# Optimization experiments

Measured on AMD Instinct MI355X. Metric: run time of the kernel, lower is better.

## Reference

```python
import jax, jax.numpy as jnp
import numpy as np

N, TI, ENC_DIM, DEC_DIM, ATT_DIM = 32, 2000, 512, 512, 512


def setup_inputs() -> dict:
    key = jax.random.key(0)
    ks = jax.random.split(key, 8)
    enc_pad = jax.random.normal(ks[0], (N, TI, ENC_DIM), dtype=jnp.float32)
    dec_prev = jax.random.normal(ks[1], (N, DEC_DIM), dtype=jnp.float32)
    ali_prev = jax.random.uniform(ks[2], (N, TI), dtype=jnp.float32)
    # lengths in [Ti//2, Ti], force one full-length row (module uses max(enc_len) as mask width)
    enc_len = jax.random.randint(ks[3], (N,), TI // 2, TI + 1)
    enc_len = enc_len.at[0].set(TI)
    # learned params (nn.Linear layout: W [out, in])
    s_e = 1.0 / np.sqrt(ENC_DIM)
    s_d = 1.0 / np.sqrt(DEC_DIM)
    s_a = 1.0 / np.sqrt(ATT_DIM)
    W_enc = jax.random.uniform(ks[4], (ATT_DIM, ENC_DIM), minval=-s_e, maxval=s_e, dtype=jnp.float32)
    b_enc = jax.random.uniform(ks[5], (ATT_DIM,), minval=-s_e, maxval=s_e, dtype=jnp.float32)
    W_dec = jax.random.uniform(ks[6], (ATT_DIM, DEC_DIM), minval=-s_d, maxval=s_d, dtype=jnp.float32)
    w_v = jax.random.uniform(ks[7], (ATT_DIM,), minval=-s_a, maxval=s_a, dtype=jnp.float32)
    return {"enc_pad": enc_pad, "enc_len": enc_len, "dec_prev": dec_prev,
            "ali_prev": ali_prev, "W_enc": W_enc, "b_enc": b_enc,
            "W_dec": W_dec, "w_v": w_v}


def reference(enc_pad, enc_len, dec_prev, ali_prev, W_enc, b_enc, W_dec, w_v):
    # enc_part: N x Ti x A  (enc_proj with bias)
    enc_part = jnp.einsum('ntd,ad->nta', enc_pad, W_enc) + b_enc
    # dec_part: N x A  (dec_proj, no bias)
    dec_part = jnp.einsum('nd,ad->na', dec_prev, W_dec)
    # additive score e = w^T tanh(enc_part + dec_part): N x Ti
    e = jnp.einsum('nta,a->nt', jnp.tanh(enc_part + dec_part[:, None, :]), w_v)
    # padding mask: positions >= enc_len are masked
    mask = jnp.arange(e.shape[1]) >= enc_len[:, None]  # N x Ti
    e = jnp.where(mask, -jnp.inf, e)
    ali = jax.nn.softmax(e, axis=1)  # N x Ti
    ctx = jnp.einsum('nt,ntd->nd', ali, enc_pad)  # N x D_enc
    return (ali, ctx)
```

## Files before the change

### kernel.cpp

```cpp
#include <hip/hip_runtime.h>
#include <stdint.h>


#define NB  32
#define TI  2000
#define ED  512
#define AD  512
#define M_TOT (NB * TI)
#define NSPLIT 20
#define TCHUNK (TI / NSPLIT)
#define MTS 500
#define NKS 16

using f16x8 = __attribute__((ext_vector_type(8))) _Float16;
using f32x4 = __attribute__((ext_vector_type(4))) float;

#define GLD16(g, l)                                                     \
    __builtin_amdgcn_global_load_lds(                                   \
        (const __attribute__((address_space(1))) void*)(g),             \
        (__attribute__((address_space(3))) void*)(l), 16, 0, 0)

__device__ __forceinline__ float fast_tanh(float s) {
    s = fminf(fmaxf(s, -15.f), 15.f);
    float t = __expf(2.f * s);
    return __fdividef(t - 1.f, t + 1.f);
}

__device__ __forceinline__ f16x8 cvt8(float4 a, float4 b) {
    f16x8 h;
    h[0] = (_Float16)a.x; h[1] = (_Float16)a.y; h[2] = (_Float16)a.z; h[3] = (_Float16)a.w;
    h[4] = (_Float16)b.x; h[5] = (_Float16)b.y; h[6] = (_Float16)b.z; h[7] = (_Float16)b.w;
    return h;
}

__global__ void k_wconvert(const float* __restrict__ Wenc, _Float16* __restrict__ W16,
                           const float* __restrict__ dec_prev, const float* __restrict__ W_dec,
                           const float* __restrict__ b_enc, float* __restrict__ db) {
    __shared__ float xd[ED];
    int bx = blockIdx.x;
    int tid = threadIdx.x;
    if (bx >= 128) {
        int n = bx - 128;
        for (int k = tid; k < ED; k += 256) xd[k] = dec_prev[n * ED + k];
        __syncthreads();
        for (int a = tid; a < AD; a += 256) {
            const float* wr = W_dec + (size_t)a * ED;
            float s = 0.f;
#pragma unroll 8
            for (int k = 0; k < ED; k += 4) {
                float4 w = *(const float4*)(wr + k);
                s += xd[k] * w.x + xd[k + 1] * w.y + xd[k + 2] * w.z + xd[k + 3] * w.w;
            }
            db[n * AD + a] = s + b_enc[a];
        }
        return;
    }
    int idx = bx * 4096 + tid * 16;
    int ks  = idx >> 15;
    int r   = idx & 32767;
    int gk  = r >> 13;
    int a   = (r & 8191) >> 4;
    int k   = ks * 32 + gk * 8;
    const float* s = Wenc + (size_t)a * ED + k;
    float4 x0 = *(const float4*)s;
    float4 x1 = *(const float4*)(s + 4);
    *(f16x8*)((char*)W16 + idx) = cvt8(x0, x1);
}

__global__ void k_decdb(const float* __restrict__ dec_prev,
                        const float* __restrict__ W_dec,
                        const float* __restrict__ b_enc,
                        float* __restrict__ db) {
    int n = blockIdx.x;
    __shared__ float xd[ED];
    for (int k = threadIdx.x; k < ED; k += 256) xd[k] = dec_prev[n * ED + k];
    __syncthreads();
    for (int a = threadIdx.x; a < AD; a += 256) {
        const float* wr = W_dec + (size_t)a * ED;
        float s = 0.f;
#pragma unroll 8
        for (int k = 0; k < ED; k += 4) {
            float4 w = *(const float4*)(wr + k);
            s += xd[k] * w.x + xd[k + 1] * w.y + xd[k + 2] * w.z + xd[k + 3] * w.w;
        }
        db[n * AD + a] = s + b_enc[a];
    }
}

__launch_bounds__(512, 2)
__global__ void k_score256(const float* __restrict__ enc, const _Float16* __restrict__ W16,
                           const float* __restrict__ db, const float* __restrict__ wv,
                           float* __restrict__ e_out) {
    __shared__ alignas(16) char As0[16384];
    __shared__ alignas(16) char As1[16384];
    __shared__ alignas(16) char Bs0[32768];
    __shared__ alignas(16) char Bs1[32768];

    const int mt   = blockIdx.x;
    const int tid  = threadIdx.x;
    const int lane = tid & 63;
    const int w    = tid >> 6;
    const int wm   = w >> 2;
    const int wn   = w & 3;
    const int m0   = mt * 128;
    const int lr   = lane & 15;
    const int gk   = lane >> 4;

    const int srow = tid >> 3;
    const int sq   = (tid & 7) * 16;
    const int sqx  = (sq ^ ((srow & 7) << 4)) >> 2;
    const float* asrc = enc + (size_t)(m0 + srow) * ED + sqx;

    const char* wbase = (const char*)W16;

    f32x4 acc[4][8];
#pragma unroll
    for (int rb = 0; rb < 4; ++rb)
#pragma unroll
        for (int cb = 0; cb < 8; ++cb) acc[rb][cb] = (f32x4){0.f, 0.f, 0.f, 0.f};

#define STAGE(ks, dA, dB)                                               \
    {                                                                   \
        GLD16(asrc + (ks) * 32,            (dA) + tid * 16);            \
        GLD16(asrc + 64 * ED + (ks) * 32,  (dA) + 8192 + tid * 16);     \
        const char* wsl = wbase + ((ks) << 15);                         \
        GLD16(wsl + tid * 16,          (dB) + tid * 16);                \
        GLD16(wsl + 8192 + tid * 16,   (dB) + 8192 + tid * 16);         \
        GLD16(wsl + 16384 + tid * 16,  (dB) + 16384 + tid * 16);        \
        GLD16(wsl + 24576 + tid * 16,  (dB) + 24576 + tid * 16);        \
    }

#define COMPUTE(sA, sB)                                                          \
    {                                                                            \
        f16x8 aF[4], bF[8];                                                      \
        _Pragma("unroll")                                                        \
        for (int rb = 0; rb < 4; ++rb) {                                         \
            int row = wm * 64 + rb * 16 + lr;                                    \
            int b0  = row * 128 + gk * 32;                                       \
            int sw  = (row & 7) << 4;                                            \
            f32x4 lo = *(const f32x4*)((sA) + (b0 ^ sw));                        \
            f32x4 hi = *(const f32x4*)((sA) + ((b0 + 16) ^ sw));                 \
            f16x8 h;                                                             \
            h[0] = (_Float16)lo[0]; h[1] = (_Float16)lo[1];                      \
            h[2] = (_Float16)lo[2]; h[3] = (_Float16)lo[3];                      \
            h[4] = (_Float16)hi[0]; h[5] = (_Float16)hi[1];                      \
            h[6] = (_Float16)hi[2]; h[7] = (_Float16)hi[3];                      \
            aF[rb] = h;                                                          \
        }                                                                        \
        _Pragma("unroll")                                                        \
        for (int cb = 0; cb < 8; ++cb) {                                         \
            int brow = wn * 128 + cb * 16 + lr;                                  \
            bF[cb] = *(const f16x8*)((sB) + gk * 8192 + brow * 16);              \
        }                                                                        \
        __builtin_amdgcn_s_setprio(1);                                           \
        _Pragma("unroll")                                                        \
        for (int rb = 0; rb < 4; ++rb)                                           \
            _Pragma("unroll")                                                    \
            for (int cb = 0; cb < 8; ++cb)                                       \
                acc[rb][cb] = __builtin_amdgcn_mfma_f32_16x16x32_f16(            \
                    aF[rb], bF[cb], acc[rb][cb], 0, 0, 0);                       \
        __builtin_amdgcn_s_setprio(0);                                           \
    }

#define ITER(k, Ac, Bc, An, Bn)  STAGE(k + 1, An, Bn); COMPUTE(Ac, Bc); __syncthreads();

    STAGE(0, As0, Bs0); __syncthreads();
    ITER(0,  As0, Bs0, As1, Bs1)
    ITER(1,  As1, Bs1, As0, Bs0)
    ITER(2,  As0, Bs0, As1, Bs1)
    ITER(3,  As1, Bs1, As0, Bs0)
    ITER(4,  As0, Bs0, As1, Bs1)
    ITER(5,  As1, Bs1, As0, Bs0)
    ITER(6,  As0, Bs0, As1, Bs1)
    ITER(7,  As1, Bs1, As0, Bs0)
    ITER(8,  As0, Bs0, As1, Bs1)
    ITER(9,  As1, Bs1, As0, Bs0)
    ITER(10, As0, Bs0, As1, Bs1)
    ITER(11, As1, Bs1, As0, Bs0)
    ITER(12, As0, Bs0, As1, Bs1)
    ITER(13, As1, Bs1, As0, Bs0)
    ITER(14, As0, Bs0, As1, Bs1)
    COMPUTE(As1, Bs1); __syncthreads();
#undef ITER
#undef COMPUTE
#undef STAGE

    float* e_red = (float*)As0;
    float wvv[8];
#pragma unroll
    for (int cb = 0; cb < 8; ++cb) wvv[cb] = wv[wn * 128 + cb * 16 + lr];

#pragma unroll
    for (int rb = 0; rb < 4; ++rb) {
#pragma unroll
        for (int i = 0; i < 4; ++i) {
            int row_local = wm * 64 + rb * 16 + gk * 4 + i;
            int m = m0 + row_local;
            int n = m / TI;
            const float* dbp = db + (size_t)n * AD + wn * 128;
            float rs = 0.f;
#pragma unroll
            for (int cb = 0; cb < 8; ++cb) {
                float s = acc[rb][cb][i] + dbp[cb * 16 + lr];
                rs += fast_tanh(s) * wvv[cb];
            }
            rs += __shfl_xor(rs, 1);
            rs += __shfl_xor(rs, 2);
            rs += __shfl_xor(rs, 4);
            rs += __shfl_xor(rs, 8);
            if (lr == 0) e_red[wn * 128 + row_local] = rs;
        }
    }
    __syncthreads();
    if (tid < 128)
        e_out[m0 + tid] =
            e_red[tid] + e_red[128 + tid] + e_red[256 + tid] + e_red[384 + tid];
}

__launch_bounds__(256, 2)
__global__ void k_score_fb(const float* __restrict__ X, const float* __restrict__ W,
                           const float* __restrict__ db, const float* __restrict__ wv,
                           float* __restrict__ e_part) {
    __shared__ alignas(16) _Float16 Xs[128][72];
    __shared__ alignas(16) _Float16 Ws[128][72];
    __shared__ float e_red[2][128];

    const int tid = threadIdx.x, lane = tid & 63, wid = tid >> 6;
    const int wr = wid >> 1, wc = wid & 1;
    const int m0 = blockIdx.x * 128, a0 = blockIdx.y * 128;

    f32x4 acc[4][4];
#pragma unroll
    for (int rb = 0; rb < 4; ++rb)
#pragma unroll
        for (int cb = 0; cb < 4; ++cb) acc[rb][cb] = (f32x4){0.f, 0.f, 0.f, 0.f};

    const int lr = lane & 15;
    const int lk = (lane >> 4) << 3;

    for (int kt = 0; kt < ED; kt += 64) {
#pragma unroll
        for (int i = 0; i < 4; ++i) {
            int idx = tid + i * 256, r = idx >> 3, c = (idx & 7) << 3;
            const float* gx = X + (size_t)(m0 + r) * ED + kt + c;
            float4 x0 = *(const float4*)gx, x1 = *(const float4*)(gx + 4);
            *(f16x8*)&Xs[r][c] = cvt8(x0, x1);
            const float* gw = W + (size_t)(a0 + r) * ED + kt + c;
            float4 w0 = *(const float4*)gw, w1 = *(const float4*)(gw + 4);
            *(f16x8*)&Ws[r][c] = cvt8(w0, w1);
        }
        __syncthreads();
#pragma unroll
        for (int kb = 0; kb < 64; kb += 32) {
            f16x8 aF[4], bF[4];
#pragma unroll
            for (int rb = 0; rb < 4; ++rb) aF[rb] = *(const f16x8*)&Xs[wr * 64 + rb * 16 + lr][kb + lk];
#pragma unroll
            for (int cb = 0; cb < 4; ++cb) bF[cb] = *(const f16x8*)&Ws[wc * 64 + cb * 16 + lr][kb + lk];
#pragma unroll
            for (int rb = 0; rb < 4; ++rb)
#pragma unroll
                for (int cb = 0; cb < 4; ++cb)
                    acc[rb][cb] = __builtin_amdgcn_mfma_f32_16x16x32_f16(aF[rb], bF[cb], acc[rb][cb], 0, 0, 0);
        }
        __syncthreads();
    }

    const int lg = lane >> 4;
    float wvv[4];
#pragma unroll
    for (int cb = 0; cb < 4; ++cb) wvv[cb] = wv[a0 + wc * 64 + cb * 16 + lr];
#pragma unroll
    for (int rb = 0; rb < 4; ++rb) {
#pragma unroll
        for (int i = 0; i < 4; ++i) {
            int row_local = wr * 64 + rb * 16 + lg * 4 + i;
            int m = m0 + row_local;
            int n = m / TI;
            const float* dbp = db + (size_t)n * AD + a0 + wc * 64;
            float rs = 0.f;
#pragma unroll
            for (int cb = 0; cb < 4; ++cb) {
                float s = acc[rb][cb][i] + dbp[cb * 16 + lr];
                rs += fast_tanh(s) * wvv[cb];
            }
            rs += __shfl_xor(rs, 1);
            rs += __shfl_xor(rs, 2);
            rs += __shfl_xor(rs, 4);
            rs += __shfl_xor(rs, 8);
            if (lr == 0) e_red[wc][row_local] = rs;
        }
    }
    __syncthreads();
    if (tid < 128)
        e_part[(size_t)blockIdx.y * M_TOT + m0 + tid] = e_red[0][tid] + e_red[1][tid];
}

__global__ void k_softmax(const float* __restrict__ e_part,
                          const int* __restrict__ enc_len,
                          float* __restrict__ ali, int nparts) {
    int n = blockIdx.x;
    int len = enc_len[n];
    __shared__ float se[TI];
    __shared__ float redm[4];
    __shared__ float reds[4];
    int tid = threadIdx.x;
    int lane = tid & 63, wid = tid >> 6;

    for (int t = tid; t < TI; t += 256) {
        float s = 0.f;
        for (int p = 0; p < nparts; ++p) s += e_part[(size_t)p * M_TOT + n * TI + t];
        se[t] = s;
    }
    __syncthreads();

    float mx = -1e30f;
    for (int t = tid; t < len; t += 256) mx = fmaxf(mx, se[t]);
#pragma unroll
    for (int o = 32; o >= 1; o >>= 1) mx = fmaxf(mx, __shfl_xor(mx, o));
    if (lane == 0) redm[wid] = mx;
    __syncthreads();
    mx = fmaxf(fmaxf(redm[0], redm[1]), fmaxf(redm[2], redm[3]));

    float sm = 0.f;
    for (int t = tid; t < len; t += 256) {
        float ex = __expf(se[t] - mx);
        se[t] = ex;
        sm += ex;
    }
#pragma unroll
    for (int o = 32; o >= 1; o >>= 1) sm += __shfl_xor(sm, o);
    if (lane == 0) reds[wid] = sm;
    __syncthreads();
    float inv = 1.f / (reds[0] + reds[1] + reds[2] + reds[3]);

    for (int t = tid; t < TI; t += 256)
        ali[n * TI + t] = (t < len) ? se[t] * inv : 0.f;
}

__global__ void k_ctxpart(const float* __restrict__ enc,
                          const float* __restrict__ ali,
                          float* __restrict__ cpart) {
    int s = blockIdx.x;
    int n = blockIdx.y;
    int d0 = threadIdx.x * 2;
    const float* base = enc + ((size_t)n * TI + s * TCHUNK) * ED + d0;
    const float* ap = ali + n * TI + s * TCHUNK;
    float ax = 0.f, ay = 0.f;
#pragma unroll 4
    for (int t = 0; t < TCHUNK; ++t) {
        float a = ap[t];
        float2 v = *(const float2*)(base + (size_t)t * ED);
        ax = fmaf(a, v.x, ax);
        ay = fmaf(a, v.y, ay);
    }
    float2 r; r.x = ax; r.y = ay;
    *(float2*)&cpart[((size_t)(n * NSPLIT + s)) * ED + d0] = r;
}

__global__ void k_ctxred(const float* __restrict__ cpart, float* __restrict__ ctx) {
    int n = blockIdx.x;
    for (int d = threadIdx.x; d < ED; d += 256) {
        float sum = 0.f;
#pragma unroll
        for (int s = 0; s < NSPLIT; ++s) sum += cpart[((size_t)(n * NSPLIT + s)) * ED + d];
        ctx[(size_t)n * ED + d] = sum;
    }
}

extern "C" void kernel_launch(void* const* d_in, const int* in_sizes, int n_in,
                              void* d_out, int out_size, void* d_ws, size_t ws_size,
                              hipStream_t stream) {
    const float* enc_pad  = (const float*)d_in[0];
    const int*   enc_len  = (const int*)d_in[1];
    const float* dec_prev = (const float*)d_in[2];
    const float* W_enc    = (const float*)d_in[4];
    const float* b_enc    = (const float*)d_in[5];
    const float* W_dec    = (const float*)d_in[6];
    const float* w_v      = (const float*)d_in[7];

    float* out = (float*)d_out;
    float* ali = out;
    float* ctx = out + M_TOT;

    float* ws     = (float*)d_ws;
    float* db     = ws;
    float* e_part = ws + NB * AD;
    float* cpart  = e_part + 4 * M_TOT;
    size_t fp_floats = (size_t)NB * AD + 4 * M_TOT + (size_t)NB * NSPLIT * ED;
    _Float16* W16 = (_Float16*)((char*)d_ws + fp_floats * 4);
    size_t need = fp_floats * 4 + (size_t)512 * 1024;
    bool big = ws_size >= need;

    if (big) {
        hipLaunchKernelGGL(k_wconvert, dim3(160), dim3(256), 0, stream,
                           W_enc, W16, dec_prev, W_dec, b_enc, db);
        hipLaunchKernelGGL(k_score256, dim3(MTS), dim3(512), 0, stream,
                           enc_pad, W16, db, w_v, e_part);
        hipLaunchKernelGGL(k_softmax, dim3(NB), dim3(256), 0, stream, e_part, enc_len, ali, 1);
    } else {
        hipLaunchKernelGGL(k_decdb, dim3(NB), dim3(256), 0, stream, dec_prev, W_dec, b_enc, db);
        hipLaunchKernelGGL(k_score_fb, dim3(M_TOT / 128, 4), dim3(256), 0, stream,
                           enc_pad, W_enc, db, w_v, e_part);
        hipLaunchKernelGGL(k_softmax, dim3(NB), dim3(256), 0, stream, e_part, enc_len, ali, 4);
    }
    hipLaunchKernelGGL(k_ctxpart, dim3(NSPLIT, NB), dim3(256), 0, stream, enc_pad, ali, cpart);
    hipLaunchKernelGGL(k_ctxred, dim3(NB), dim3(256), 0, stream, cpart, ctx);
}
```

Measured before the change: 119.9 us.

## Triple-buffer the score GEMM K-loop with explicit vmcnt waits

```diff
diff --git a/kernel.cpp b/kernel.cpp
--- a/kernel.cpp
+++ b/kernel.cpp
@@ -93,8 +93,10 @@
                            float* __restrict__ e_out) {
     __shared__ alignas(16) char As0[16384];
     __shared__ alignas(16) char As1[16384];
+    __shared__ alignas(16) char As2[16384];
     __shared__ alignas(16) char Bs0[32768];
     __shared__ alignas(16) char Bs1[32768];
+    __shared__ alignas(16) char Bs2[32768];
 
     const int mt   = blockIdx.x;
     const int tid  = threadIdx.x;
@@ -162,28 +164,37 @@
         __builtin_amdgcn_s_setprio(0);                                           \
     }
 
-#define ITER(k, Ac, Bc, An, Bn)  STAGE(k + 1, An, Bn); COMPUTE(Ac, Bc); __syncthreads();
-
-    STAGE(0, As0, Bs0); __syncthreads();
-    ITER(0,  As0, Bs0, As1, Bs1)
-    ITER(1,  As1, Bs1, As0, Bs0)
-    ITER(2,  As0, Bs0, As1, Bs1)
-    ITER(3,  As1, Bs1, As0, Bs0)
-    ITER(4,  As0, Bs0, As1, Bs1)
-    ITER(5,  As1, Bs1, As0, Bs0)
-    ITER(6,  As0, Bs0, As1, Bs1)
-    ITER(7,  As1, Bs1, As0, Bs0)
-    ITER(8,  As0, Bs0, As1, Bs1)
-    ITER(9,  As1, Bs1, As0, Bs0)
-    ITER(10, As0, Bs0, As1, Bs1)
-    ITER(11, As1, Bs1, As0, Bs0)
-    ITER(12, As0, Bs0, As1, Bs1)
-    ITER(13, As1, Bs1, As0, Bs0)
-    ITER(14, As0, Bs0, As1, Bs1)
-    COMPUTE(As1, Bs1); __syncthreads();
-#undef ITER
+#define WAITV(N)                                                        \
+    asm volatile("s_waitcnt vmcnt(" #N ")" ::: "memory");               \
+    __builtin_amdgcn_sched_barrier(0)
+#define BAR __builtin_amdgcn_s_barrier()
+
+    STAGE(0, As0, Bs0);
+    STAGE(1, As1, Bs1);
+    STAGE(2, As2, Bs2);
+
+    WAITV(12); BAR; COMPUTE(As0, Bs0); BAR; STAGE(3,  As0, Bs0);
+    WAITV(12); BAR; COMPUTE(As1, Bs1); BAR; STAGE(4,  As1, Bs1);
+    WAITV(12); BAR; COMPUTE(As2, Bs2); BAR; STAGE(5,  As2, Bs2);
+    WAITV(12); BAR; COMPUTE(As0, Bs0); BAR; STAGE(6,  As0, Bs0);
+    WAITV(12); BAR; COMPUTE(As1, Bs1); BAR; STAGE(7,  As1, Bs1);
+    WAITV(12); BAR; COMPUTE(As2, Bs2); BAR; STAGE(8,  As2, Bs2);
+    WAITV(12); BAR; COMPUTE(As0, Bs0); BAR; STAGE(9,  As0, Bs0);
+    WAITV(12); BAR; COMPUTE(As1, Bs1); BAR; STAGE(10, As1, Bs1);
+    WAITV(12); BAR; COMPUTE(As2, Bs2); BAR; STAGE(11, As2, Bs2);
+    WAITV(12); BAR; COMPUTE(As0, Bs0); BAR; STAGE(12, As0, Bs0);
+    WAITV(12); BAR; COMPUTE(As1, Bs1); BAR; STAGE(13, As1, Bs1);
+    WAITV(12); BAR; COMPUTE(As2, Bs2); BAR; STAGE(14, As2, Bs2);
+    WAITV(12); BAR; COMPUTE(As0, Bs0); BAR; STAGE(15, As0, Bs0);
+    WAITV(12); BAR; COMPUTE(As1, Bs1); BAR;
+    WAITV(6);  BAR; COMPUTE(As2, Bs2); BAR;
+    WAITV(0);  BAR; COMPUTE(As0, Bs0);
+#undef WAITV
+#undef BAR
 #undef COMPUTE
 #undef STAGE
+
+    __syncthreads();
 
     float* e_red = (float*)As0;
     float wvv[8];
```

Result: slower. 124.8 us (+4.1%).
